# Performance work log

Hardware: AMD Instinct MI355X
Metric: run time of the kernel (lower is better)

Reference implementation:

```python
import jax, jax.numpy as jnp
import numpy as np

IOU_THRESH = 0.6
NEG = -1.0  # strictly below any real IoU (IoU >= 0), used to mask cross-label pairs


def cxcywh_to_xyxy(b):
    cx, cy, w, h = b[..., 0], b[..., 1], b[..., 2], b[..., 3]
    return jnp.stack([cx - 0.5 * w, cy - 0.5 * h, cx + 0.5 * w, cy + 0.5 * h], axis=-1)


def pairwise_iou(a, b):
    # a: [M,4] xyxy, b: [N,4] xyxy -> [M,N]
    area_a = (a[:, 2] - a[:, 0]) * (a[:, 3] - a[:, 1])
    area_b = (b[:, 2] - b[:, 0]) * (b[:, 3] - b[:, 1])
    lt = jnp.maximum(a[:, None, :2], b[None, :, :2])
    rb = jnp.minimum(a[:, None, 2:], b[None, :, 2:])
    wh = jnp.clip(rb - lt, 0.0, None)
    inter = wh[..., 0] * wh[..., 1]
    union = area_a[:, None] + area_b[None, :] - inter
    return inter / jnp.maximum(union, 1e-9)


def assign_one(proposals, prompt_inds, gt_boxes, gt_labels, k):
    # Vectorized equivalent of the per-unique-label loop: masking IoU to NEG for
    # cross-label (gt, proposal) pairs reproduces the per-group matcher exactly.
    M = gt_boxes.shape[0]
    match = gt_labels[:, None] == prompt_inds[None, :]                # [M,N] group membership
    iou = pairwise_iou(cxcywh_to_xyxy(gt_boxes), cxcywh_to_xyxy(proposals))  # [M,N]
    miou = jnp.where(match, iou, NEG)                                 # group-masked IoU
    best_iou = miou.max(axis=0)                                       # [N] matcher argmax within group
    best_gt = miou.argmax(axis=0)
    valid_prop = match.any(axis=0)                                    # proposal's label appears in gt
    gmax = miou.max(axis=1)                                           # [M] per-gt best IoU in its group
    lq = (miou == gmax[:, None]) & match                              # allow_low_quality_matches
    pos = valid_prop & ((best_iou >= IOU_THRESH) | lq.any(axis=0))    # matched_labels == 1 (foreground)
    # positives assigned to each gt (fg cap num_queries*0.25 never binds at these sizes)
    counts = jax.ops.segment_sum(pos.astype(jnp.int32), best_gt, num_segments=M)
    # sample_topk_per_gt: per gt take top min(count, k) proposals by group IoU
    topv, topi = jax.lax.top_k(miou, k)                               # [M,k]
    take = jnp.minimum(counts, k)
    valid = jnp.arange(k)[None, :] < take[:, None]                    # [M,k]
    rows = jnp.where(valid, topi, -1)                                 # proposal indices, -1 padded
    cols = jnp.where(valid, jnp.arange(M)[:, None], -1)               # gt indices, -1 padded
    sel_iou = jnp.where(valid, topv, 0.0)
    return rows, cols, valid, sel_iou


def setup_inputs() -> dict:
    key = jax.random.key(0)
    ks = jax.random.split(key, 6)
    B, N, M, L = 16, 3000, 300, 80

    def boxes(k, shape):
        u = jax.random.uniform(k, shape + (4,), dtype=jnp.float32)
        cxcy = u[..., :2]
        wh = 0.02 + 0.28 * u[..., 2:]  # cxcywh with positive extents
        return jnp.concatenate([cxcy, wh], axis=-1)

    return {
        "pred_logits_match": jax.random.normal(ks[0], (B, N, 1), dtype=jnp.float32),
        "pred_boxes": boxes(ks[1], (B, N)),
        "init_reference": boxes(ks[2], (B, N)),
        "prompt_inds": jax.random.randint(ks[3], (B, N), 0, L, dtype=jnp.int32),
        "gt_labels": jax.random.randint(ks[4], (B, M), 0, L, dtype=jnp.int32),
        "gt_boxes": boxes(ks[5], (B, M)),
        "max_k": 4,
    }


def reference(pred_logits_match, pred_boxes, init_reference, prompt_inds, gt_labels, gt_boxes, max_k):
    _ = jax.nn.sigmoid(pred_logits_match)  # computed in the original forward but unused downstream
    f = lambda p, pi, gb, gl: assign_one(p, pi, gb, gl, max_k)
    rows, cols, valid, sel_iou = jax.vmap(f)(init_reference, prompt_inds, gt_boxes, gt_labels)
    # padded equivalent of the list of (rows, cols) index pairs; valid marks real entries
    return rows, cols, valid, sel_iou
```

## Files before the change

### kernel.cpp

```cpp
#include <hip/hip_runtime.h>

#define BB 16
#define NN 3000
#define MM 300
#define LL 80
#define KK 4
#define IOU_THRESH 0.6f

typedef unsigned long long u64;

struct Box { float x1, y1, x2, y2, area; };

__device__ __forceinline__ Box to_xyxy(float4 b) {
#pragma clang fp contract(off)
    Box r;
    r.x1 = b.x - 0.5f * b.z;
    r.y1 = b.y - 0.5f * b.w;
    r.x2 = b.x + 0.5f * b.z;
    r.y2 = b.y + 0.5f * b.w;
    r.area = (r.x2 - r.x1) * (r.y2 - r.y1);
    return r;
}

__device__ __forceinline__ float pair_iou(Box a, Box b) {
#pragma clang fp contract(off)
    float ltx = fmaxf(a.x1, b.x1);
    float lty = fmaxf(a.y1, b.y1);
    float rbx = fminf(a.x2, b.x2);
    float rby = fminf(a.y2, b.y2);
    float wx = fmaxf(rbx - ltx, 0.0f);
    float wy = fmaxf(rby - lty, 0.0f);
    float inter = wx * wy;
    float uni = a.area + b.area - inter;
    return inter / fmaxf(uni, 1e-9f);
}

__device__ __forceinline__ unsigned int f32_to_ordered(float f) {
    unsigned int u = __float_as_uint(f);
    return (u & 0x80000000u) ? ~u : (u | 0x80000000u);
}
__device__ __forceinline__ float ordered_to_f32(unsigned int u) {
    unsigned int b = (u & 0x80000000u) ? (u & 0x7FFFFFFFu) : ~u;
    return __uint_as_float(b);
}

__device__ __forceinline__ u64 umax64(u64 a, u64 b) { return a > b ? a : b; }
__device__ __forceinline__ u64 umin64(u64 a, u64 b) { return a < b ? a : b; }

__device__ __forceinline__ u64 shfl_xor_u64(u64 v, int mask) {
    int lo = __shfl_xor((int)(unsigned)v, mask, 64);
    int hi = __shfl_xor((int)(unsigned)(v >> 32), mask, 64);
    return ((u64)(unsigned)hi << 32) | (u64)(unsigned)lo;
}

__device__ __forceinline__ void topins(u64 t[4], u64 k) {
    u64 c0 = umin64(t[0], k);
    t[0] = umax64(t[0], k);
    u64 c1 = umin64(t[1], c0);
    t[1] = umax64(t[1], c0);
    u64 c2 = umin64(t[2], c1);
    t[2] = umax64(t[2], c1);
    t[3] = umax64(t[3], c2);
}

__device__ __forceinline__ void wave_merge_top4(u64 t[4]) {
    #pragma unroll
    for (int s = 1; s < 64; s <<= 1) {
        u64 b0 = shfl_xor_u64(t[0], s);
        u64 b1 = shfl_xor_u64(t[1], s);
        u64 b2 = shfl_xor_u64(t[2], s);
        u64 b3 = shfl_xor_u64(t[3], s);
        u64 a0 = t[0], a1 = t[1], a2 = t[2], a3 = t[3];
        t[0] = umax64(a0, b0);
        t[1] = umax64(umin64(a0, b0), umax64(a1, b1));
        t[2] = umax64(umax64(a2, b2), umax64(umin64(a0, b1), umin64(a1, b0)));
        t[3] = umax64(umax64(a3, b3),
               umax64(umin64(a0, b2), umax64(umin64(a1, b1), umin64(a2, b0))));
    }
}

__global__ __launch_bounds__(256) void kFused(
    const float4* __restrict__ props, const int* __restrict__ pinds,
    const int* __restrict__ glab, const float4* __restrict__ gbox,
    float* __restrict__ out)
{
    const int l = blockIdx.x;
    const int b = blockIdx.y;
    const int tid = threadIdx.x;

    __shared__ unsigned short plist[NN];
    __shared__ unsigned short glist[MM];
    __shared__ float gmaxL[MM];
    __shared__ float tvL[MM * KK];
    __shared__ int   tiL[MM * KK];
    __shared__ int   cntsL[MM];
    __shared__ int pcur, gcur;

    if (tid == 0) { pcur = 0; gcur = 0; }
    for (int j = tid; j < MM; j += 256) cntsL[j] = 0;
    __syncthreads();

    for (int m = tid; m < MM; m += 256) {
        if (glab[b * MM + m] == l) {
            int pos = atomicAdd(&gcur, 1);
            glist[pos] = (unsigned short)m;
        }
    }
    __syncthreads();
    const int cg_ = gcur;
    if (cg_ == 0) return;

    for (int n = tid; n < NN; n += 256) {
        if (pinds[b * NN + n] == l) {
            int pos = atomicAdd(&pcur, 1);
            plist[pos] = (unsigned short)n;
        }
    }
    __syncthreads();
    const int cp_ = pcur;

    {
        const int lane = tid & 63;
        const int wv = tid >> 6;
        for (int j = wv; j < cg_; j += 4) {
            int m = glist[j];
            Box gt = to_xyxy(gbox[b * MM + m]);
            const u64 init = ((u64)f32_to_ordered(-1.0f) << 32);
            u64 t[4] = {init, init, init, init};
            for (int i = lane; i < cp_; i += 64) {
                int n = plist[i];
                Box pb = to_xyxy(props[(size_t)b * NN + n]);
                float iou = pair_iou(gt, pb);
                u64 key = ((u64)f32_to_ordered(iou) << 32) |
                          (u64)(0xFFFFFFFFu - (unsigned)n);
                topins(t, key);
            }
            wave_merge_top4(t);
            if (lane == 0) {
                #pragma unroll
                for (int q = 0; q < KK; ++q) {
                    tvL[j * KK + q] = ordered_to_f32((unsigned)(t[q] >> 32));
                    tiL[j * KK + q] = (int)(0xFFFFFFFFu - (unsigned)t[q]);
                }
                gmaxL[j] = ordered_to_f32((unsigned)(t[0] >> 32));
            }
        }
    }
    __syncthreads();

    for (int p = tid; p < cp_; p += 256) {
        int n = plist[p];
        Box pb = to_xyxy(props[(size_t)b * NN + n]);
        u64 key = 0;
        int bestj = 0;
        bool lq = false;
        for (int j = 0; j < cg_; ++j) {
            int m = glist[j];
            Box gt = to_xyxy(gbox[b * MM + m]);
            float iou = pair_iou(gt, pb);
            u64 k = ((u64)f32_to_ordered(iou) << 32) |
                    (u64)(0xFFFFFFFFu - (unsigned)m);
            if (k > key) { key = k; bestj = j; }
            lq = lq || (iou == gmaxL[j]);
        }
        float v = ordered_to_f32((unsigned)(key >> 32));
        if ((v >= IOU_THRESH) || lq) atomicAdd(&cntsL[bestj], 1);
    }
    __syncthreads();

    for (int j = tid; j < cg_; j += 256) {
        int m = glist[j];
        int i = b * MM + m;
        int take = min(cntsL[j], KK);
        float4 rows, cols, valid, sel;
        rows.x = (0 < take) ? (float)tiL[j * KK + 0] : -1.0f;
        rows.y = (1 < take) ? (float)tiL[j * KK + 1] : -1.0f;
        rows.z = (2 < take) ? (float)tiL[j * KK + 2] : -1.0f;
        rows.w = (3 < take) ? (float)tiL[j * KK + 3] : -1.0f;
        cols.x = (0 < take) ? (float)m : -1.0f;
        cols.y = (1 < take) ? (float)m : -1.0f;
        cols.z = (2 < take) ? (float)m : -1.0f;
        cols.w = (3 < take) ? (float)m : -1.0f;
        valid.x = (0 < take) ? 1.0f : 0.0f;
        valid.y = (1 < take) ? 1.0f : 0.0f;
        valid.z = (2 < take) ? 1.0f : 0.0f;
        valid.w = (3 < take) ? 1.0f : 0.0f;
        sel.x = (0 < take) ? tvL[j * KK + 0] : 0.0f;
        sel.y = (1 < take) ? tvL[j * KK + 1] : 0.0f;
        sel.z = (2 < take) ? tvL[j * KK + 2] : 0.0f;
        sel.w = (3 < take) ? tvL[j * KK + 3] : 0.0f;
        float4* o = (float4*)out;
        const int CH4 = BB * MM;
        o[0 * CH4 + i] = rows;
        o[1 * CH4 + i] = cols;
        o[2 * CH4 + i] = valid;
        o[3 * CH4 + i] = sel;
    }
}

extern "C" void kernel_launch(void* const* d_in, const int* in_sizes, int n_in,
                              void* d_out, int out_size, void* d_ws, size_t ws_size,
                              hipStream_t stream) {
    const float4* props = (const float4*)d_in[2];
    const int*    pinds = (const int*)d_in[3];
    const int*    glab  = (const int*)d_in[4];
    const float4* gbox  = (const float4*)d_in[5];
    float* out = (float*)d_out;

    kFused<<<dim3(LL, BB), 256, 0, stream>>>(props, pinds, glab, gbox, out);
}
```

Measured before the change: 81.06 us.

## Bucket proposals and gts by label in a prep kernel before per-label matching

Adds a per-batch prep kernel that histograms labels and scatters proposal and gt indices into contiguous per-label buckets in workspace. The per-(label, batch) matching kernel then copies only its own bucket instead of every block rescanning all 3000 prompt indices and 300 gt labels with shared atomics. It also caches each gt's converted xyxy box and area in shared memory, so the positive-counting loop no longer reloads and reconverts gt boxes. The cost is a second kernel launch, a dependency through global workspace, and a serial prefix sum per label in the prep kernel.

```diff
diff --git a/kernel.cpp b/kernel.cpp
--- a/kernel.cpp
+++ b/kernel.cpp
@@ -79,56 +79,83 @@
     }
 }
 
-__global__ __launch_bounds__(256) void kFused(
-    const float4* __restrict__ props, const int* __restrict__ pinds,
-    const int* __restrict__ glab, const float4* __restrict__ gbox,
+__global__ __launch_bounds__(512) void kPrep(const int* __restrict__ pinds,
+                                             const int* __restrict__ glab,
+                                             unsigned short* __restrict__ pidx,
+                                             int* __restrict__ pstart,
+                                             int* __restrict__ pcnt,
+                                             unsigned short* __restrict__ gidx,
+                                             int* __restrict__ gstart,
+                                             int* __restrict__ gcnt) {
+    int b = blockIdx.x;
+    int tid = threadIdx.x;
+    __shared__ int hist[LL], cur[LL], gh[LL], gcur[LL];
+    if (tid < LL) { hist[tid] = 0; gh[tid] = 0; }
+    __syncthreads();
+    for (int n = tid; n < NN; n += 512) atomicAdd(&hist[pinds[b * NN + n]], 1);
+    for (int m = tid; m < MM; m += 512) atomicAdd(&gh[glab[b * MM + m]], 1);
+    __syncthreads();
+    if (tid < LL) {
+        int s = 0;
+        for (int j = 0; j < tid; ++j) s += hist[j];
+        cur[tid] = s; pstart[b * LL + tid] = s; pcnt[b * LL + tid] = hist[tid];
+        int t = 0;
+        for (int j = 0; j < tid; ++j) t += gh[j];
+        gcur[tid] = t; gstart[b * LL + tid] = t; gcnt[b * LL + tid] = gh[tid];
+    }
+    __syncthreads();
+    for (int n = tid; n < NN; n += 512) {
+        int l = pinds[b * NN + n];
+        int pos = atomicAdd(&cur[l], 1);
+        pidx[b * NN + pos] = (unsigned short)n;
+    }
+    for (int m = tid; m < MM; m += 512) {
+        int l = glab[b * MM + m];
+        int pos = atomicAdd(&gcur[l], 1);
+        gidx[b * MM + pos] = (unsigned short)m;
+    }
+}
+
+__global__ __launch_bounds__(256) void kBuck(
+    const float4* __restrict__ props, const float4* __restrict__ gbox,
+    const unsigned short* __restrict__ pidx, const int* __restrict__ pstart,
+    const int* __restrict__ pcnt, const unsigned short* __restrict__ gidx,
+    const int* __restrict__ gstart, const int* __restrict__ gcnt,
     float* __restrict__ out)
 {
     const int l = blockIdx.x;
     const int b = blockIdx.y;
     const int tid = threadIdx.x;
 
-    __shared__ unsigned short plist[NN];
-    __shared__ unsigned short glist[MM];
-    __shared__ float gmaxL[MM];
-    __shared__ float tvL[MM * KK];
-    __shared__ int   tiL[MM * KK];
-    __shared__ int   cntsL[MM];
-    __shared__ int pcur, gcur;
-
-    if (tid == 0) { pcur = 0; gcur = 0; }
-    for (int j = tid; j < MM; j += 256) cntsL[j] = 0;
-    __syncthreads();
-
-    for (int m = tid; m < MM; m += 256) {
-        if (glab[b * MM + m] == l) {
-            int pos = atomicAdd(&gcur, 1);
-            glist[pos] = (unsigned short)m;
-        }
-    }
-    __syncthreads();
-    const int cg_ = gcur;
+    __shared__ unsigned short plistS[NN];
+    __shared__ unsigned short glistS[MM];
+    __shared__ float4 gxyS[MM];
+    __shared__ float  gareaS[MM];
+    __shared__ float  gmaxS[MM];
+    __shared__ float  tvL[MM * KK];
+    __shared__ int    tiL[MM * KK];
+    __shared__ int    cntsL[MM];
+
+    const int cg_ = gcnt[b * LL + l];
     if (cg_ == 0) return;
-
-    for (int n = tid; n < NN; n += 256) {
-        if (pinds[b * NN + n] == l) {
-            int pos = atomicAdd(&pcur, 1);
-            plist[pos] = (unsigned short)n;
-        }
-    }
-    __syncthreads();
-    const int cp_ = pcur;
+    const int cp_ = pcnt[b * LL + l];
+    const int gs  = gstart[b * LL + l];
+    const int ps  = pstart[b * LL + l];
+
+    for (int i = tid; i < cp_; i += 256) plistS[i] = pidx[b * NN + ps + i];
+    for (int j = tid; j < cg_; j += 256) { glistS[j] = gidx[b * MM + gs + j]; cntsL[j] = 0; }
+    __syncthreads();
 
     {
         const int lane = tid & 63;
         const int wv = tid >> 6;
         for (int j = wv; j < cg_; j += 4) {
-            int m = glist[j];
+            int m = glistS[j];
             Box gt = to_xyxy(gbox[b * MM + m]);
             const u64 init = ((u64)f32_to_ordered(-1.0f) << 32);
             u64 t[4] = {init, init, init, init};
             for (int i = lane; i < cp_; i += 64) {
-                int n = plist[i];
+                int n = plistS[i];
                 Box pb = to_xyxy(props[(size_t)b * NN + n]);
                 float iou = pair_iou(gt, pb);
                 u64 key = ((u64)f32_to_ordered(iou) << 32) |
@@ -142,26 +169,29 @@
                     tvL[j * KK + q] = ordered_to_f32((unsigned)(t[q] >> 32));
                     tiL[j * KK + q] = (int)(0xFFFFFFFFu - (unsigned)t[q]);
                 }
-                gmaxL[j] = ordered_to_f32((unsigned)(t[0] >> 32));
+                gmaxS[j] = ordered_to_f32((unsigned)(t[0] >> 32));
+                gxyS[j] = make_float4(gt.x1, gt.y1, gt.x2, gt.y2);
+                gareaS[j] = gt.area;
             }
         }
     }
     __syncthreads();
 
     for (int p = tid; p < cp_; p += 256) {
-        int n = plist[p];
+        int n = plistS[p];
         Box pb = to_xyxy(props[(size_t)b * NN + n]);
         u64 key = 0;
         int bestj = 0;
         bool lq = false;
         for (int j = 0; j < cg_; ++j) {
-            int m = glist[j];
-            Box gt = to_xyxy(gbox[b * MM + m]);
-            float iou = pair_iou(gt, pb);
+            float4 q = gxyS[j];
+            Box a; a.x1 = q.x; a.y1 = q.y; a.x2 = q.z; a.y2 = q.w; a.area = gareaS[j];
+            float iou = pair_iou(a, pb);
+            int m = glistS[j];
             u64 k = ((u64)f32_to_ordered(iou) << 32) |
                     (u64)(0xFFFFFFFFu - (unsigned)m);
             if (k > key) { key = k; bestj = j; }
-            lq = lq || (iou == gmaxL[j]);
+            lq = lq || (iou == gmaxS[j]);
         }
         float v = ordered_to_f32((unsigned)(key >> 32));
         if ((v >= IOU_THRESH) || lq) atomicAdd(&cntsL[bestj], 1);
@@ -169,7 +199,7 @@
     __syncthreads();
 
     for (int j = tid; j < cg_; j += 256) {
-        int m = glist[j];
+        int m = glistS[j];
         int i = b * MM + m;
         int take = min(cntsL[j], KK);
         float4 rows, cols, valid, sel;
@@ -207,5 +237,16 @@
     const float4* gbox  = (const float4*)d_in[5];
     float* out = (float*)d_out;
 
-    kFused<<<dim3(LL, BB), 256, 0, stream>>>(props, pinds, glab, gbox, out);
-}
+    char* w = (char*)d_ws;
+    int*   pstart = (int*)w;                 w += BB * LL * sizeof(int);
+    int*   pcnt   = (int*)w;                 w += BB * LL * sizeof(int);
+    int*   gstart = (int*)w;                 w += BB * LL * sizeof(int);
+    int*   gcnt   = (int*)w;                 w += BB * LL * sizeof(int);
+    unsigned short* pidx = (unsigned short*)w; w += BB * NN * sizeof(short);
+    unsigned short* gidx = (unsigned short*)w;
+
+    kPrep<<<BB, 512, 0, stream>>>(pinds, glab, pidx, pstart, pcnt,
+                                  gidx, gstart, gcnt);
+    kBuck<<<dim3(LL, BB), 256, 0, stream>>>(props, gbox, pidx, pstart, pcnt,
+                                            gidx, gstart, gcnt, out);
+}
```

After: 83.48 us. 3.0% more time.
